# Optimization experiments

Hardware: AMD Instinct MI355X
Metric: run time of the kernel (lower is better)

The kernel has to match this reference:

```python
import jax, jax.numpy as jnp
import numpy as np

IMG = 128          # image_size
TEX = 4            # texture_size (hard-coded in module)
WIDTH = float(np.tan(np.radians(30.0)))  # nr default viewing_angle=30
NEAR = 0.1
# images dict: values are [distance, azimuth, elevation]; eye = get_points_from_angles(dist, elev, azim)
VIEWS = [(2.83, 45.0, 0.0), (2.0, 0.0, 90.0), (3.46, 45.0, 45.0), (3.0, 0.0, 0.0)]  # (dist, elev, azim)


def _eye_from_angles(dist, elev_deg, azim_deg):
    e, a = np.radians(elev_deg), np.radians(azim_deg)
    return jnp.asarray([dist * np.cos(e) * np.sin(a), dist * np.sin(e), -dist * np.cos(e) * np.cos(a)], jnp.float32)


def _normalize(v):
    return v / jnp.linalg.norm(v)


def _trilinear(tex, c):
    # tex: [P, T, T, T, 3], c: [P, 3] continuous coords in [0, T-1]
    i0 = jnp.clip(jnp.floor(c).astype(jnp.int32), 0, TEX - 2)
    f = c - i0.astype(c.dtype)
    pi = jnp.arange(tex.shape[0])
    out = jnp.zeros((tex.shape[0], 3), tex.dtype)
    for dx in (0, 1):
        for dy in (0, 1):
            for dz in (0, 1):
                wgt = ((f[:, 0] if dx else 1.0 - f[:, 0])
                       * (f[:, 1] if dy else 1.0 - f[:, 1])
                       * (f[:, 2] if dz else 1.0 - f[:, 2]))
                out = out + wgt[:, None] * tex[pi, i0[:, 0] + dx, i0[:, 1] + dy, i0[:, 2] + dz]
    return out


def _render(verts, faces, tex, eye):
    # verts [V,3], faces [F,3] int, tex [F,T,T,T,3] -> image [1,3,IMG,IMG]
    # look_at transform (at=origin, up=+y)
    z_ax = _normalize(-eye)
    x_ax = _normalize(jnp.cross(jnp.asarray([0.0, 1.0, 0.0], jnp.float32), z_ax))
    y_ax = _normalize(jnp.cross(z_ax, x_ax))
    R = jnp.stack([x_ax, y_ax, z_ax])                       # [3,3]
    v = (verts - eye) @ R.T                                 # [V,3]
    # perspective projection
    z = v[:, 2]
    v = jnp.stack([v[:, 0] / (z * WIDTH), v[:, 1] / (z * WIDTH), z], -1)
    fv = v[faces]                                           # [F,3,3]

    # pixel grid in NDC [-1,1], row 0 = top
    s = (jnp.arange(IMG, dtype=jnp.float32) + 0.5) / IMG * 2.0 - 1.0
    px = jnp.broadcast_to(s[None, :], (IMG, IMG)).ravel()
    py = jnp.broadcast_to(-s[:, None], (IMG, IMG)).ravel()
    p = jnp.stack([px, py], -1)                             # [P,2]

    v0 = fv[:, 0, :2]
    e1 = fv[:, 1, :2] - v0
    e2 = fv[:, 2, :2] - v0
    det = e1[:, 0] * e2[:, 1] - e1[:, 1] * e2[:, 0]         # [F]
    ok = jnp.abs(det) > 1e-8
    inv_det = jnp.where(ok, 1.0 / jnp.where(ok, det, 1.0), 0.0)
    d = p[None, :, :] - v0[:, None, :]                      # [F,P,2]
    w1 = (e2[:, None, 1] * d[..., 0] - e2[:, None, 0] * d[..., 1]) * inv_det[:, None]
    w2 = (-e1[:, None, 1] * d[..., 0] + e1[:, None, 0] * d[..., 1]) * inv_det[:, None]
    w0 = 1.0 - w1 - w2
    fz = fv[:, :, 2]                                        # [F,3]
    depth = w0 * fz[:, 0:1] + w1 * fz[:, 1:2] + w2 * fz[:, 2:3]  # [F,P]
    visible = (w0 >= 0) & (w1 >= 0) & (w2 >= 0) & ok[:, None] & (depth > NEAR)
    depth_m = jnp.where(visible, depth, jnp.inf)
    fidx = jnp.argmin(depth_m, axis=0)                      # [P]
    P = fidx.shape[0]
    pi = jnp.arange(P)
    hit = jnp.isfinite(depth_m[fidx, pi])
    wsel = jnp.stack([w0[fidx, pi], w1[fidx, pi], w2[fidx, pi]], -1)  # [P,3]
    coords = jnp.clip(wsel, 0.0, 1.0) * (TEX - 1)
    color = _trilinear(tex[fidx], coords) * hit[:, None].astype(tex.dtype)  # [P,3]
    return color.reshape(IMG, IMG, 3).transpose(2, 0, 1)[None]  # [1,3,IMG,IMG]


def setup_inputs() -> dict:
    key = jax.random.key(0)
    k1, k2, k3, k4 = jax.random.split(key, 4)
    V, F = 1024, 1024
    vertices = jax.random.normal(k1, (1, V, 3), jnp.float32) * 0.5
    faces = jax.random.randint(k2, (1, F, 3), 0, V, jnp.int32)
    textures = jax.random.normal(k3, (1, F, TEX, TEX, TEX, 3), jnp.float32)
    image_refs = jax.random.uniform(k4, (4, 1, IMG, IMG), jnp.float32)
    return {"vertices": vertices, "faces": faces, "textures": textures, "image_refs": image_refs}


def reference(vertices, faces, textures, image_refs):
    tex = jnp.tanh(textures)[0]   # [F,T,T,T,3]
    verts = vertices[0]
    fcs = faces[0]
    loss = jnp.float32(0.0)
    for c, (dist, elev, azim) in enumerate(VIEWS):
        image = _render(verts, fcs, tex, _eye_from_angles(dist, elev, azim))  # [1,3,H,W]
        ref = image_refs[c][:, None]                                          # [1,1,H,W]
        loss = loss + jnp.sum((image - ref) ** 2)
    return loss
```

## Files before the change

kernel.cpp:

```cpp
#include <hip/hip_runtime.h>
#include <math.h>

#define IMG 128
#define NPIX (IMG * IMG)
#define NF 1024
#define NCHUNK 8
#define CHF (NF / NCHUNK)
#define FSTRIDE 12
#define NEAR_Z 0.1f
#define NSHADE_BLK 256

struct AllViews { float m[4][12]; };

__global__ void precompute_faces(const float* __restrict__ verts,
                                 const int* __restrict__ faces,
                                 float* __restrict__ fd,
                                 AllViews vc, float W)
{
    int t = blockIdx.x * blockDim.x + threadIdx.x;
    if (t >= 4 * NF) return;
    int view = t >> 10, f = t & (NF - 1);
    const float* M = vc.m[view];

    float proj[3][3];
    for (int k = 0; k < 3; ++k) {
        int vi = faces[f * 3 + k];
        float px = verts[vi * 3 + 0] - M[9];
        float py = verts[vi * 3 + 1] - M[10];
        float pz = verts[vi * 3 + 2] - M[11];
        float x = M[0] * px + M[1] * py + M[2] * pz;
        float y = M[3] * px + M[4] * py + M[5] * pz;
        float z = M[6] * px + M[7] * py + M[8] * pz;
        proj[k][0] = x / (z * W);
        proj[k][1] = y / (z * W);
        proj[k][2] = z;
    }
    float v0x = proj[0][0], v0y = proj[0][1];
    float e1x = proj[1][0] - v0x, e1y = proj[1][1] - v0y;
    float e2x = proj[2][0] - v0x, e2y = proj[2][1] - v0y;
    float det = e1x * e2y - e1y * e2x;
    bool ok = fabsf(det) > 1e-8f;
    float inv = ok ? 1.0f / det : 0.0f;

    float a1x = e2y * inv, a1y = -e2x * inv;
    float b1 = -(a1x * v0x + a1y * v0y);
    float a2x = -e1y * inv, a2y = e1x * inv;
    float b2 = -(a2x * v0x + a2y * v0y);
    float g1 = proj[1][2] - proj[0][2];
    float g2 = proj[2][2] - proj[0][2];
    float ddx = g1 * a1x + g2 * a2x;
    float ddy = g1 * a1y + g2 * a2y;
    float dc  = proj[0][2] + g1 * b1 + g2 * b2;
    if (!ok) dc = 0.0f;

    float* o = fd + (size_t)(view * NF + f) * FSTRIDE;
    o[0] = a1x; o[1] = a1y; o[2] = b1;  o[3] = a2x;
    o[4] = a2y; o[5] = b2;  o[6] = ddx; o[7] = ddy;
    o[8] = dc;  o[9] = 0.0f; o[10] = 0.0f; o[11] = 0.0f;
}

__global__ __launch_bounds__(256) void raster(
    const float* __restrict__ fd,
    unsigned long long* __restrict__ keys)
{
    __shared__ float4 lds4[CHF * 3];

    int bid = blockIdx.x;
    int view  = bid >> 9;
    int b     = bid & 511;
    int chunk = b & (NCHUNK - 1);
    int ptile = b >> 3;
    int tid = threadIdx.x;

    const float4* src = (const float4*)fd + (size_t)(view * NF + chunk * CHF) * 3;
    for (int i = tid; i < CHF * 3; i += 256) lds4[i] = src[i];
    __syncthreads();

    int p = ptile * 256 + tid;
    int row = p >> 7, col = p & 127;
    float sx = ((col + 0.5f) * (1.0f / IMG)) * 2.0f - 1.0f;
    float sy = -(((row + 0.5f) * (1.0f / IMG)) * 2.0f - 1.0f);

    float best = INFINITY;
    int bf = 0;
    const float* ldsf = (const float*)lds4;

#pragma unroll 4
    for (int f = 0; f < CHF; ++f) {
        float4 Q0 = lds4[f * 3 + 0];
        float4 Q1 = lds4[f * 3 + 1];
        float dc  = ldsf[f * 12 + 8];
        float w1 = fmaf(Q0.x, sx, fmaf(Q0.y, sy, Q0.z));
        float w2 = fmaf(Q0.w, sx, fmaf(Q1.x, sy, Q1.y));
        float dep = fmaf(Q1.z, sx, fmaf(Q1.w, sy, dc));
        float s = w1 + w2;
        bool vis = (fminf(w1, w2) >= 0.0f) && (s <= 1.0f) && (dep > NEAR_Z);
        bool take = vis && (dep < best);
        best = take ? dep : best;
        bf   = take ? f : bf;
    }

    unsigned int dbits = __float_as_uint(best);
    unsigned long long key =
        ((unsigned long long)dbits << 32) |
        (unsigned int)(chunk * CHF + bf);
    keys[((size_t)(view * NCHUNK + chunk) << 14) + p] = key;
}

__global__ __launch_bounds__(256) void shade_loss(
    const float* __restrict__ fd,
    const unsigned long long* __restrict__ keys,
    const float* __restrict__ tex,
    const float* __restrict__ refs,
    float* __restrict__ partial)
{
    __shared__ float wsum[4];
    int t = blockIdx.x * blockDim.x + threadIdx.x;
    int view = t >> 14, p = t & (NPIX - 1);
    int row = p >> 7, col = p & 127;
    float sx = ((col + 0.5f) * (1.0f / IMG)) * 2.0f - 1.0f;
    float sy = -(((row + 0.5f) * (1.0f / IMG)) * 2.0f - 1.0f);

    const unsigned long long* kb = keys + ((size_t)(view * NCHUNK) << 14) + p;
    unsigned long long key = ~0ULL;
#pragma unroll
    for (int c = 0; c < NCHUNK; ++c) {
        unsigned long long k = kb[(size_t)c << 14];
        key = (k < key) ? k : key;
    }

    bool hit = (unsigned int)(key >> 32) < 0x7f800000u;
    float ref = refs[t];
    float lossv;
    if (hit) {
        int f = (int)(key & 0xffffffffu);
        const float4* Q = (const float4*)fd + (size_t)(view * NF + f) * 3;
        float4 Q0 = Q[0];
        float4 Q1 = Q[1];
        float w1 = fmaf(Q0.x, sx, fmaf(Q0.y, sy, Q0.z));
        float w2 = fmaf(Q0.w, sx, fmaf(Q1.x, sy, Q1.y));
        float w0 = 1.0f - w1 - w2;
        float cx = fminf(fmaxf(w0, 0.0f), 1.0f) * 3.0f;
        float cy = fminf(fmaxf(w1, 0.0f), 1.0f) * 3.0f;
        float cz = fminf(fmaxf(w2, 0.0f), 1.0f) * 3.0f;
        int ix = min(max((int)floorf(cx), 0), 2);
        int iy = min(max((int)floorf(cy), 0), 2);
        int iz = min(max((int)floorf(cz), 0), 2);
        float fx = cx - (float)ix, fy = cy - (float)iy, fz = cz - (float)iz;

        const float* T = tex + (size_t)f * 192;
        float c0 = 0.0f, c1 = 0.0f, c2 = 0.0f;
        for (int dxi = 0; dxi < 2; ++dxi)
            for (int dyi = 0; dyi < 2; ++dyi)
                for (int dzi = 0; dzi < 2; ++dzi) {
                    float w = (dxi ? fx : 1.0f - fx) *
                              (dyi ? fy : 1.0f - fy) *
                              (dzi ? fz : 1.0f - fz);
                    int base = (((ix + dxi) * 4 + (iy + dyi)) * 4 + (iz + dzi)) * 3;
                    c0 += w * tanhf(T[base + 0]);
                    c1 += w * tanhf(T[base + 1]);
                    c2 += w * tanhf(T[base + 2]);
                }
        float d0 = c0 - ref, d1 = c1 - ref, d2 = c2 - ref;
        lossv = d0 * d0 + d1 * d1 + d2 * d2;
    } else {
        lossv = 3.0f * ref * ref;
    }

    for (int off = 32; off; off >>= 1) lossv += __shfl_down(lossv, off);
    int tid = threadIdx.x;
    if ((tid & 63) == 0) wsum[tid >> 6] = lossv;
    __syncthreads();
    if (tid == 0) partial[blockIdx.x] = wsum[0] + wsum[1] + wsum[2] + wsum[3];
}

__global__ __launch_bounds__(256) void final_reduce(
    const float* __restrict__ partial, float* __restrict__ out)
{
    __shared__ float wsum[4];
    int tid = threadIdx.x;
    float v = partial[tid];
    for (int off = 32; off; off >>= 1) v += __shfl_down(v, off);
    if ((tid & 63) == 0) wsum[tid >> 6] = v;
    __syncthreads();
    if (tid == 0) out[0] = wsum[0] + wsum[1] + wsum[2] + wsum[3];
}

static void make_view(double dist, double elev, double azim, float* M)
{
    double e = elev * M_PI / 180.0, a = azim * M_PI / 180.0;
    float ex = (float)(dist * cos(e) * sin(a));
    float ey = (float)(dist * sin(e));
    float ez = (float)(-dist * cos(e) * cos(a));
    float zx = -ex, zy = -ey, zz = -ez;
    float n = sqrtf(zx * zx + zy * zy + zz * zz);
    zx /= n; zy /= n; zz /= n;
    float xx = zz, xy = 0.0f, xz = -zx;
    n = sqrtf(xx * xx + xy * xy + xz * xz);
    xx /= n; xy /= n; xz /= n;
    float yx = zy * xz - zz * xy;
    float yy = zz * xx - zx * xz;
    float yz = zx * xy - zy * xx;
    n = sqrtf(yx * yx + yy * yy + yz * yz);
    yx /= n; yy /= n; yz /= n;
    M[0] = xx; M[1] = xy; M[2] = xz;
    M[3] = yx; M[4] = yy; M[5] = yz;
    M[6] = zx; M[7] = zy; M[8] = zz;
    M[9] = ex; M[10] = ey; M[11] = ez;
}

extern "C" void kernel_launch(void* const* d_in, const int* in_sizes, int n_in,
                              void* d_out, int out_size, void* d_ws, size_t ws_size,
                              hipStream_t stream)
{
    const float* verts = (const float*)d_in[0];
    const int*   faces = (const int*)d_in[1];
    const float* tex   = (const float*)d_in[2];
    const float* refs  = (const float*)d_in[3];
    float* out = (float*)d_out;

    char* ws = (char*)d_ws;
    float* fd = (float*)ws;
    ws += 4 * NF * FSTRIDE * sizeof(float);
    unsigned long long* keys = (unsigned long long*)ws;
    ws += (size_t)4 * NCHUNK * NPIX * sizeof(unsigned long long);
    float* partial = (float*)ws;

    AllViews vc;
    const double V[4][3] = {{2.83, 45.0, 0.0}, {2.0, 0.0, 90.0},
                            {3.46, 45.0, 45.0}, {3.0, 0.0, 0.0}};
    for (int i = 0; i < 4; ++i) make_view(V[i][0], V[i][1], V[i][2], vc.m[i]);
    float W = (float)tan(M_PI / 6.0);

    precompute_faces<<<16, 256, 0, stream>>>(verts, faces, fd, vc, W);
    raster<<<2048, 256, 0, stream>>>(fd, keys);
    shade_loss<<<NSHADE_BLK, 256, 0, stream>>>(fd, keys, tex, refs, partial);
    final_reduce<<<1, 256, 0, stream>>>(partial, out);
}
```

Before: 45.94 us.

## Fuse face projection into raster and shade kernels, add bounding-box culling

Removes the separate face precompute kernel: each raster block projects its 128-face chunk into LDS, and shade_loss recomputes the plane equations for the winning face. The raster loop also skips a face when its screen bounding box misses the wavefront's row and half-row column span. This drops one kernel launch and the face-data buffer round trip, and cuts per-pixel edge tests. In exchange, projection work is repeated in every raster block and in every shade thread that hits a face, and the skip branch can diverge within a wavefront.

```diff
diff --git a/kernel.cpp b/kernel.cpp
--- a/kernel.cpp
+++ b/kernel.cpp
@@ -5,24 +5,17 @@
 #define NPIX (IMG * IMG)
 #define NF 1024
 #define NCHUNK 8
-#define CHF (NF / NCHUNK)
-#define FSTRIDE 12
+#define CHF 128
 #define NEAR_Z 0.1f
 #define NSHADE_BLK 256
 
 struct AllViews { float m[4][12]; };
 
-__global__ void precompute_faces(const float* __restrict__ verts,
-                                 const int* __restrict__ faces,
-                                 float* __restrict__ fd,
-                                 AllViews vc, float W)
-{
-    int t = blockIdx.x * blockDim.x + threadIdx.x;
-    if (t >= 4 * NF) return;
-    int view = t >> 10, f = t & (NF - 1);
-    const float* M = vc.m[view];
-
-    float proj[3][3];
+__device__ __forceinline__ void project_face(
+    const float* __restrict__ verts, const int* __restrict__ faces,
+    const float* M, float W, int f, float proj[3][3])
+{
+#pragma unroll
     for (int k = 0; k < 3; ++k) {
         int vi = faces[f * 3 + k];
         float px = verts[vi * 3 + 0] - M[9];
@@ -35,35 +28,38 @@
         proj[k][1] = y / (z * W);
         proj[k][2] = z;
     }
+}
+
+__device__ __forceinline__ void face_planes(const float proj[3][3],
+    float& a1x, float& a1y, float& b1, float& a2x, float& a2y, float& b2,
+    float& ddx, float& ddy, float& dc)
+{
     float v0x = proj[0][0], v0y = proj[0][1];
     float e1x = proj[1][0] - v0x, e1y = proj[1][1] - v0y;
     float e2x = proj[2][0] - v0x, e2y = proj[2][1] - v0y;
     float det = e1x * e2y - e1y * e2x;
     bool ok = fabsf(det) > 1e-8f;
     float inv = ok ? 1.0f / det : 0.0f;
-
-    float a1x = e2y * inv, a1y = -e2x * inv;
-    float b1 = -(a1x * v0x + a1y * v0y);
-    float a2x = -e1y * inv, a2y = e1x * inv;
-    float b2 = -(a2x * v0x + a2y * v0y);
+    a1x = e2y * inv; a1y = -e2x * inv;
+    b1 = -(a1x * v0x + a1y * v0y);
+    a2x = -e1y * inv; a2y = e1x * inv;
+    b2 = -(a2x * v0x + a2y * v0y);
     float g1 = proj[1][2] - proj[0][2];
     float g2 = proj[2][2] - proj[0][2];
-    float ddx = g1 * a1x + g2 * a2x;
-    float ddy = g1 * a1y + g2 * a2y;
-    float dc  = proj[0][2] + g1 * b1 + g2 * b2;
+    ddx = g1 * a1x + g2 * a2x;
+    ddy = g1 * a1y + g2 * a2y;
+    dc  = proj[0][2] + g1 * b1 + g2 * b2;
     if (!ok) dc = 0.0f;
-
-    float* o = fd + (size_t)(view * NF + f) * FSTRIDE;
-    o[0] = a1x; o[1] = a1y; o[2] = b1;  o[3] = a2x;
-    o[4] = a2y; o[5] = b2;  o[6] = ddx; o[7] = ddy;
-    o[8] = dc;  o[9] = 0.0f; o[10] = 0.0f; o[11] = 0.0f;
 }
 
 __global__ __launch_bounds__(256) void raster(
-    const float* __restrict__ fd,
-    unsigned long long* __restrict__ keys)
-{
-    __shared__ float4 lds4[CHF * 3];
+    const float* __restrict__ verts, const int* __restrict__ faces,
+    unsigned long long* __restrict__ keys, AllViews vc, float W)
+{
+    __shared__ float4 BB[CHF];
+    __shared__ float4 P0[CHF];
+    __shared__ float4 P1[CHF];
+    __shared__ float  DC[CHF];
 
     int bid = blockIdx.x;
     int view  = bid >> 9;
@@ -72,29 +68,44 @@
     int ptile = b >> 3;
     int tid = threadIdx.x;
 
-    const float4* src = (const float4*)fd + (size_t)(view * NF + chunk * CHF) * 3;
-    for (int i = tid; i < CHF * 3; i += 256) lds4[i] = src[i];
+    if (tid < CHF) {
+        int f = chunk * CHF + tid;
+        float proj[3][3];
+        project_face(verts, faces, vc.m[view], W, f, proj);
+        float a1x, a1y, b1, a2x, a2y, b2, ddx, ddy, dc;
+        face_planes(proj, a1x, a1y, b1, a2x, a2y, b2, ddx, ddy, dc);
+        P0[tid] = make_float4(a1x, a1y, b1, a2x);
+        P1[tid] = make_float4(a2y, b2, ddx, ddy);
+        DC[tid] = dc;
+        float ymin = fminf(fminf(proj[0][1], proj[1][1]), proj[2][1]);
+        float ymax = fmaxf(fmaxf(proj[0][1], proj[1][1]), proj[2][1]);
+        float xmin = fminf(fminf(proj[0][0], proj[1][0]), proj[2][0]);
+        float xmax = fmaxf(fmaxf(proj[0][0], proj[1][0]), proj[2][0]);
+        BB[tid] = make_float4(ymin, ymax, xmin, xmax);
+    }
     __syncthreads();
 
     int p = ptile * 256 + tid;
     int row = p >> 7, col = p & 127;
-    float sx = ((col + 0.5f) * (1.0f / IMG)) * 2.0f - 1.0f;
-    float sy = -(((row + 0.5f) * (1.0f / IMG)) * 2.0f - 1.0f);
+    float sx = (col + 0.5f) * (2.0f / IMG) - 1.0f;
+    float sy = -((row + 0.5f) * (2.0f / IMG) - 1.0f);
+    int col0 = tid & 64;
+    float wx0 = (col0 + 0.5f) * (2.0f / IMG) - 1.0f;
+    float wx1 = (col0 + 63.5f) * (2.0f / IMG) - 1.0f;
 
     float best = INFINITY;
     int bf = 0;
-    const float* ldsf = (const float*)lds4;
-
-#pragma unroll 4
+
     for (int f = 0; f < CHF; ++f) {
-        float4 Q0 = lds4[f * 3 + 0];
-        float4 Q1 = lds4[f * 3 + 1];
-        float dc  = ldsf[f * 12 + 8];
-        float w1 = fmaf(Q0.x, sx, fmaf(Q0.y, sy, Q0.z));
-        float w2 = fmaf(Q0.w, sx, fmaf(Q1.x, sy, Q1.y));
+        float4 bb = BB[f];
+        if (bb.x > sy || bb.y < sy || bb.z > wx1 || bb.w < wx0) continue;
+        float4 Q0 = P0[f];
+        float4 Q1 = P1[f];
+        float dc  = DC[f];
+        float w1  = fmaf(Q0.x, sx, fmaf(Q0.y, sy, Q0.z));
+        float w2  = fmaf(Q0.w, sx, fmaf(Q1.x, sy, Q1.y));
         float dep = fmaf(Q1.z, sx, fmaf(Q1.w, sy, dc));
-        float s = w1 + w2;
-        bool vis = (fminf(w1, w2) >= 0.0f) && (s <= 1.0f) && (dep > NEAR_Z);
+        bool vis  = (fminf(w1, w2) >= 0.0f) && (w1 + w2 <= 1.0f) && (dep > NEAR_Z);
         bool take = vis && (dep < best);
         best = take ? dep : best;
         bf   = take ? f : bf;
@@ -102,24 +113,23 @@
 
     unsigned int dbits = __float_as_uint(best);
     unsigned long long key =
-        ((unsigned long long)dbits << 32) |
-        (unsigned int)(chunk * CHF + bf);
+        ((unsigned long long)dbits << 32) | (unsigned int)(chunk * CHF + bf);
     keys[((size_t)(view * NCHUNK + chunk) << 14) + p] = key;
 }
 
 __global__ __launch_bounds__(256) void shade_loss(
-    const float* __restrict__ fd,
+    const float* __restrict__ verts, const int* __restrict__ faces,
     const unsigned long long* __restrict__ keys,
     const float* __restrict__ tex,
     const float* __restrict__ refs,
-    float* __restrict__ partial)
+    float* __restrict__ partial, AllViews vc, float W)
 {
     __shared__ float wsum[4];
     int t = blockIdx.x * blockDim.x + threadIdx.x;
     int view = t >> 14, p = t & (NPIX - 1);
     int row = p >> 7, col = p & 127;
-    float sx = ((col + 0.5f) * (1.0f / IMG)) * 2.0f - 1.0f;
-    float sy = -(((row + 0.5f) * (1.0f / IMG)) * 2.0f - 1.0f);
+    float sx = (col + 0.5f) * (2.0f / IMG) - 1.0f;
+    float sy = -((row + 0.5f) * (2.0f / IMG) - 1.0f);
 
     const unsigned long long* kb = keys + ((size_t)(view * NCHUNK) << 14) + p;
     unsigned long long key = ~0ULL;
@@ -134,11 +144,12 @@
     float lossv;
     if (hit) {
         int f = (int)(key & 0xffffffffu);
-        const float4* Q = (const float4*)fd + (size_t)(view * NF + f) * 3;
-        float4 Q0 = Q[0];
-        float4 Q1 = Q[1];
-        float w1 = fmaf(Q0.x, sx, fmaf(Q0.y, sy, Q0.z));
-        float w2 = fmaf(Q0.w, sx, fmaf(Q1.x, sy, Q1.y));
+        float proj[3][3];
+        project_face(verts, faces, vc.m[view], W, f, proj);
+        float a1x, a1y, b1, a2x, a2y, b2, ddx, ddy, dc;
+        face_planes(proj, a1x, a1y, b1, a2x, a2y, b2, ddx, ddy, dc);
+        float w1 = fmaf(a1x, sx, fmaf(a1y, sy, b1));
+        float w2 = fmaf(a2x, sx, fmaf(a2y, sy, b2));
         float w0 = 1.0f - w1 - w2;
         float cx = fminf(fmaxf(w0, 0.0f), 1.0f) * 3.0f;
         float cy = fminf(fmaxf(w1, 0.0f), 1.0f) * 3.0f;
@@ -220,8 +231,6 @@
     float* out = (float*)d_out;
 
     char* ws = (char*)d_ws;
-    float* fd = (float*)ws;
-    ws += 4 * NF * FSTRIDE * sizeof(float);
     unsigned long long* keys = (unsigned long long*)ws;
     ws += (size_t)4 * NCHUNK * NPIX * sizeof(unsigned long long);
     float* partial = (float*)ws;
@@ -232,8 +241,8 @@
     for (int i = 0; i < 4; ++i) make_view(V[i][0], V[i][1], V[i][2], vc.m[i]);
     float W = (float)tan(M_PI / 6.0);
 
-    precompute_faces<<<16, 256, 0, stream>>>(verts, faces, fd, vc, W);
-    raster<<<2048, 256, 0, stream>>>(fd, keys);
-    shade_loss<<<NSHADE_BLK, 256, 0, stream>>>(fd, keys, tex, refs, partial);
+    raster<<<2048, 256, 0, stream>>>(verts, faces, keys, vc, W);
+    shade_loss<<<NSHADE_BLK, 256, 0, stream>>>(verts, faces, keys, tex, refs,
+                                               partial, vc, W);
     final_reduce<<<1, 256, 0, stream>>>(partial, out);
 }
```

Measured after the change: 46.67 us. Within noise of the previous version (+1.6%).
